# Performance work log

Measured on AMD Instinct MI355X. Metric: run time of the kernel, lower is better.

The kernel has to match this reference:

```python
import jax, jax.numpy as jnp
import numpy as np

E, D, H, TOP_K = 6, 256, 256, 2
ROUTER_H = D // 2  # 128


def setup_inputs() -> dict:
    key = jax.random.key(0)
    ks = jax.random.split(key, 12)
    s = 1.0 / np.sqrt(D)
    sh = 1.0 / np.sqrt(H)
    sr = 1.0 / np.sqrt(ROUTER_H)
    return {
        "features": jax.random.normal(ks[0], (8, 4096, D), dtype=jnp.float32),
        "router_w1": jax.random.uniform(ks[1], (D, ROUTER_H), jnp.float32, -s, s),
        "router_b1": jnp.zeros((ROUTER_H,), jnp.float32),
        "router_w2": jax.random.uniform(ks[2], (ROUTER_H, E), jnp.float32, -sr, sr),
        "router_b2": jnp.zeros((E,), jnp.float32),
        "expert_w1": jax.random.uniform(ks[3], (E, D, H), jnp.float32, -s, s),
        "expert_b1": jnp.zeros((E, H), jnp.float32),
        "expert_w2": jax.random.uniform(ks[4], (E, H, H), jnp.float32, -sh, sh),
        "expert_b2": jnp.zeros((E, H), jnp.float32),
        "expert_w3": jax.random.uniform(ks[5], (E, H, D), jnp.float32, -sh, sh),
        "expert_b3": jnp.zeros((E, D), jnp.float32),
    }


def reference(features, router_w1, router_b1, router_w2, router_b2,
              expert_w1, expert_b1, expert_w2, expert_b2, expert_w3, expert_b3):
    # ---- Router: Linear -> ReLU -> Linear -> Softmax, then top-k + renormalizing softmax
    rh = jax.nn.relu(features @ router_w1 + router_b1)          # [B,S,128]
    expert_logits = jax.nn.softmax(rh @ router_w2 + router_b2, axis=-1)  # [B,S,E]
    top_w, top_i = jax.lax.top_k(expert_logits, TOP_K)          # [B,S,K]
    routing_weights = jax.nn.softmax(top_w, axis=-1)            # [B,S,K]

    # ---- Run ALL experts over all tokens (dense, as in the original)
    h1 = jax.nn.relu(jnp.einsum('bsd,edh->bseh', features, expert_w1) + expert_b1)   # [B,S,E,H]
    h2 = jax.nn.relu(jnp.einsum('bseh,ehf->bsef', h1, expert_w2) + expert_b2)        # [B,S,E,H]
    expert_out = jnp.einsum('bsef,efo->bseo', h2, expert_w3) + expert_b3             # [B,S,E,D]

    # ---- Gather top-k expert outputs and combine with routing weights
    sel = jnp.take_along_axis(expert_out, top_i[:, :, :, None], axis=2)  # [B,S,K,D]
    combined = jnp.sum(sel * routing_weights[..., None], axis=2)         # [B,S,D]
    return combined
```

## Files before the change

### kernel.cpp

```cpp
#include <hip/hip_runtime.h>


#define N_TOK 32768
#define E_EXP 6

typedef _Float16 f16x8 __attribute__((ext_vector_type(8)));
typedef float    f32x4 __attribute__((ext_vector_type(4)));
typedef unsigned int u32x4 __attribute__((ext_vector_type(4)));

#define WS_LIST 256
#define WS_WA   (WS_LIST + 15 * N_TOK * 4)
#define WS_WT   (WS_WA + 15 * N_TOK * 4)
#define WS_R1H  (WS_WT + 2359296)
#define WS_R1L  (WS_R1H + 131072)

__device__ __forceinline__ unsigned pack_f16x2(float x, float y) {
  unsigned short a = __builtin_bit_cast(unsigned short, (_Float16)x);
  unsigned short b = __builtin_bit_cast(unsigned short, (_Float16)y);
  return (unsigned)a | ((unsigned)b << 16);
}

__device__ __forceinline__ void split_pair(float x, float y,
                                           unsigned& hi, unsigned& lo) {
  _Float16 xh = (_Float16)x, yh = (_Float16)y;
  float xl = (x - (float)xh) * 2048.f, yl = (y - (float)yh) * 2048.f;
  hi = (unsigned)__builtin_bit_cast(unsigned short, xh) |
       ((unsigned)__builtin_bit_cast(unsigned short, yh) << 16);
  lo = pack_f16x2(xl, yl);
}

__global__ __launch_bounds__(256) void convert_w_kernel(
    const float* __restrict__ w1, const float* __restrict__ w2,
    const float* __restrict__ w3, const float* __restrict__ rw1,
    _Float16* __restrict__ wt, _Float16* __restrict__ r1h,
    _Float16* __restrict__ r1l, int* __restrict__ counts) {
  __shared__ __align__(16) float xs[32 * 256];
  int blk = blockIdx.x;
  int t = threadIdx.x;
  if (blk == 0 && t < 16) counts[t] = 0;
  float4* xs4 = (float4*)xs;
  if (blk < 144) {
    int kt = blk & 7, el = blk >> 3, l = el % 3, e = el / 3;
    const float* W = (l == 0 ? w1 : (l == 1 ? w2 : w3)) +
                     (size_t)e * 65536 + (size_t)kt * 32 * 256;
    const float4* s4 = (const float4*)W;
    #pragma unroll
    for (int j = 0; j < 8; ++j) xs4[j * 256 + t] = s4[j * 256 + t];
    __syncthreads();
    _Float16* dst = wt + ((size_t)(e * 3 + l) * 8 + kt) * 8192;
    #pragma unroll
    for (int si = 0; si < 4; ++si) {
      int S = si * 256 + t;
      int Ls = S & 63;
      int n = ((S >> 6) << 4) + (Ls & 15);
      int qq = Ls >> 4;
      u32x4 pk;
      #pragma unroll
      for (int i = 0; i < 4; ++i) {
        float x = xs[(qq * 8 + 2 * i) * 256 + n];
        float y = xs[(qq * 8 + 2 * i + 1) * 256 + n];
        pk[i] = pack_f16x2(x, y);
      }
      *(u32x4*)(dst + S * 8) = pk;
    }
  } else {
    int kt = blk - 144;
    const float4* s4 = (const float4*)(rw1 + (size_t)kt * 32 * 128);
    #pragma unroll
    for (int j = 0; j < 4; ++j) xs4[j * 256 + t] = s4[j * 256 + t];
    __syncthreads();
    #pragma unroll
    for (int si = 0; si < 2; ++si) {
      int S = si * 256 + t;
      int Ls = S & 63;
      int n = ((S >> 6) << 4) + (Ls & 15);
      int qq = Ls >> 4;
      u32x4 ph, pl;
      #pragma unroll
      for (int i = 0; i < 4; ++i) {
        float x = xs[(qq * 8 + 2 * i) * 128 + n];
        float y = xs[(qq * 8 + 2 * i + 1) * 128 + n];
        unsigned hi, lo;
        split_pair(x, y, hi, lo);
        ph[i] = hi; pl[i] = lo;
      }
      size_t off = (size_t)kt * 4096 + S * 8;
      *(u32x4*)(r1h + off) = ph;
      *(u32x4*)(r1l + off) = pl;
    }
  }
}

__global__ __launch_bounds__(256) void router_kernel(
    const float* __restrict__ feat, const _Float16* __restrict__ r1h,
    const _Float16* __restrict__ r1l, const float* __restrict__ rb1,
    const float* __restrict__ rw2, const float* __restrict__ rb2,
    int* __restrict__ counts, int* __restrict__ list,
    float* __restrict__ wA) {
  __shared__ __align__(16) char smem[65536];
  __shared__ float plg[64 * 25];
  __shared__ int lcnt[15], gbase[15];
  _Float16* Ahi = (_Float16*)smem;
  _Float16* Alo = (_Float16*)(smem + 32768);
  float* rh = (float*)smem;

  int tid = threadIdx.x;
  int wv = tid >> 6, L = tid & 63, m = L & 15, q = L >> 4;
  int tok0 = blockIdx.x * 64;

  {
    int row = tid >> 2, seg = tid & 3;
    int rt = row >> 4, mm = row & 15;
    const float4* src = (const float4*)(feat + (size_t)(tok0 + row) * 256 + seg * 64);
    #pragma unroll
    for (int i = 0; i < 8; ++i) {
      float4 a = src[2 * i], b = src[2 * i + 1];
      u32x4 ph, pl;
      unsigned h0, l0;
      split_pair(a.x, a.y, h0, l0); ph[0] = h0; pl[0] = l0;
      split_pair(a.z, a.w, h0, l0); ph[1] = h0; pl[1] = l0;
      split_pair(b.x, b.y, h0, l0); ph[2] = h0; pl[2] = l0;
      split_pair(b.z, b.w, h0, l0); ph[3] = h0; pl[3] = l0;
      int k = seg * 64 + i * 8;
      int off = (((k >> 5) * 4 + rt) * 64 + ((k >> 3) & 3) * 16 + mm) * 8;
      *(u32x4*)(Ahi + off) = ph;
      *(u32x4*)(Alo + off) = pl;
    }
  }
  if (tid < 15) lcnt[tid] = 0;

  auto ldH = [&](int kt, int ct) -> f16x8 {
    return *(const f16x8*)(r1h + ((kt * 8 + wv * 2 + ct) * 64 + L) * 8);
  };
  auto ldL = [&](int kt, int ct) -> f16x8 {
    return *(const f16x8*)(r1l + ((kt * 8 + wv * 2 + ct) * 64 + L) * 8);
  };
  f16x8 bch[2], bcl[2];
  #pragma unroll
  for (int ct = 0; ct < 2; ++ct) { bch[ct] = ldH(0, ct); bcl[ct] = ldL(0, ct); }
  __syncthreads();

  f32x4 ach[4][2], acm[4][2];
  #pragma unroll
  for (int ct = 0; ct < 2; ++ct) {
    float bv = rb1[wv * 32 + ct * 16 + m];
    #pragma unroll
    for (int rt = 0; rt < 4; ++rt) {
      ach[rt][ct][0] = bv; ach[rt][ct][1] = bv;
      ach[rt][ct][2] = bv; ach[rt][ct][3] = bv;
      acm[rt][ct][0] = 0.f; acm[rt][ct][1] = 0.f;
      acm[rt][ct][2] = 0.f; acm[rt][ct][3] = 0.f;
    }
  }
  #pragma unroll
  for (int kt = 0; kt < 8; ++kt) {
    f16x8 bnh[2], bnl[2];
    if (kt < 7) {
      #pragma unroll
      for (int ct = 0; ct < 2; ++ct) { bnh[ct] = ldH(kt + 1, ct); bnl[ct] = ldL(kt + 1, ct); }
    }
    f16x8 ah[4], al[4];
    #pragma unroll
    for (int rt = 0; rt < 4; ++rt) {
      ah[rt] = *(const f16x8*)(Ahi + ((kt * 4 + rt) * 64 + L) * 8);
      al[rt] = *(const f16x8*)(Alo + ((kt * 4 + rt) * 64 + L) * 8);
    }
    #pragma unroll
    for (int rt = 0; rt < 4; ++rt)
      #pragma unroll
      for (int ct = 0; ct < 2; ++ct)
        ach[rt][ct] = __builtin_amdgcn_mfma_f32_16x16x32_f16(
            ah[rt], bch[ct], ach[rt][ct], 0, 0, 0);
    #pragma unroll
    for (int rt = 0; rt < 4; ++rt)
      #pragma unroll
      for (int ct = 0; ct < 2; ++ct) {
        acm[rt][ct] = __builtin_amdgcn_mfma_f32_16x16x32_f16(
            ah[rt], bcl[ct], acm[rt][ct], 0, 0, 0);
        acm[rt][ct] = __builtin_amdgcn_mfma_f32_16x16x32_f16(
            al[rt], bch[ct], acm[rt][ct], 0, 0, 0);
      }
    if (kt < 7) {
      #pragma unroll
      for (int ct = 0; ct < 2; ++ct) { bch[ct] = bnh[ct]; bcl[ct] = bnl[ct]; }
    }
  }
  __syncthreads();

  #pragma unroll
  for (int rt = 0; rt < 4; ++rt)
    #pragma unroll
    for (int ct = 0; ct < 2; ++ct)
      #pragma unroll
      for (int r = 0; r < 4; ++r) {
        float v = ach[rt][ct][r] + acm[rt][ct][r] * (1.f / 2048.f);
        int row = rt * 16 + q * 4 + r, h = wv * 32 + ct * 16 + m;
        rh[row * 132 + h] = fmaxf(v, 0.f);
      }
  __syncthreads();

  {
    int t = tid >> 2, sub = tid & 3;
    float lgp[E_EXP] = {0.f, 0.f, 0.f, 0.f, 0.f, 0.f};
    #pragma unroll
    for (int c = 0; c < 8; ++c) {
      int c4 = sub * 8 + c;
      float4 xv = *(const float4*)(rh + t * 132 + c4 * 4);
      #pragma unroll
      for (int j = 0; j < 4; ++j) {
        float xj = (j == 0) ? xv.x : (j == 1) ? xv.y : (j == 2) ? xv.z : xv.w;
        const float* wr = rw2 + (c4 * 4 + j) * E_EXP;
        #pragma unroll
        for (int e2 = 0; e2 < E_EXP; ++e2)
          lgp[e2] = fmaf(xj, wr[e2], lgp[e2]);
      }
    }
    float* pp = plg + t * 25 + sub * 6;
    #pragma unroll
    for (int e2 = 0; e2 < E_EXP; ++e2) pp[e2] = lgp[e2];
  }
  __syncthreads();

  int pid = 0, loc = 0, token = 0;
  float wa = 0.f;
  if (tid < 64) {
    token = tok0 + tid;
    float p[E_EXP];
    float mx = -1e30f;
    #pragma unroll
    for (int i = 0; i < E_EXP; ++i) {
      p[i] = rb2[i] + plg[tid * 25 + i] + plg[tid * 25 + 6 + i] +
             plg[tid * 25 + 12 + i] + plg[tid * 25 + 18 + i];
      mx = fmaxf(mx, p[i]);
    }
    float sum = 0.f;
    #pragma unroll
    for (int i = 0; i < E_EXP; ++i) { p[i] = expf(p[i] - mx); sum += p[i]; }
    float inv = 1.f / sum;
    #pragma unroll
    for (int i = 0; i < E_EXP; ++i) p[i] *= inv;
    float b1v = p[0]; int sel0 = 0;
    #pragma unroll
    for (int i = 1; i < E_EXP; ++i) if (p[i] > b1v) { b1v = p[i]; sel0 = i; }
    float b2v = -1.f; int sel1 = 0;
    #pragma unroll
    for (int i = 0; i < E_EXP; ++i)
      if (i != sel0 && p[i] > b2v) { b2v = p[i]; sel1 = i; }
    float r = expf(b2v - b1v);
    float sw0 = 1.f / (1.f + r);
    float sw1 = r / (1.f + r);
    int a = sel0 < sel1 ? sel0 : sel1;
    int b = sel0 < sel1 ? sel1 : sel0;
    wa = (sel0 < sel1) ? sw0 : sw1;
    pid = b * (b - 1) / 2 + a;
    loc = atomicAdd(&lcnt[pid], 1);
  }
  __syncthreads();
  if (tid < 15) gbase[tid] = atomicAdd(&counts[tid], lcnt[tid]);
  __syncthreads();
  if (tid < 64) {
    int p0 = gbase[pid] + loc;
    list[pid * N_TOK + p0] = token;
    wA[pid * N_TOK + p0] = wa;
  }
}

__global__ __launch_bounds__(256) void expert_kernel(
    const float* __restrict__ feat, const _Float16* __restrict__ wt,
    const float* __restrict__ eb1, const float* __restrict__ eb2,
    const float* __restrict__ eb3, const int* __restrict__ counts,
    const int* __restrict__ list, const float* __restrict__ wA,
    float* __restrict__ out) {
  __shared__ __align__(16) _Float16 Ah[8192];
  __shared__ int   toks[32];
  __shared__ float wgA[32];

  const int loT[15] = {0,0,1,0,1,2,0,1,2,3,0,1,2,3,4};
  const int hiT[15] = {1,2,2,3,3,3,4,4,4,4,5,5,5,5,5};

  int bid = blockIdx.x;
  int pid = 0, tile = 0, cnt = 0, cum = 0;
  #pragma unroll
  for (int i = 0; i < 15; ++i) {
    int ci = counts[i];
    int nt = (ci + 31) >> 5;
    bool hit = (bid >= cum) && (bid < cum + nt);
    if (hit) { pid = i; tile = bid - cum; cnt = ci; }
    cum += nt;
  }
  if (bid >= cum) return;
  int base = tile * 32;
  int eLo = loT[pid], eHi = hiT[pid];

  int tid = threadIdx.x;
  int wv = tid >> 6, L = tid & 63, m = L & 15, q = L >> 4;
  int wcol = wv * 64;

  if (tid < 32) {
    int idx = base + tid;
    int tk = 0; float a = 0.f;
    if (idx < cnt) { tk = list[pid * N_TOK + idx]; a = wA[pid * N_TOK + idx]; }
    toks[tid] = tk; wgA[tid] = a;
  }

  auto ldBs = [&](int s, int ct) -> f16x8 {
    int ee = (s >= 24) ? eHi : eLo;
    int ss = (s >= 24) ? s - 24 : s;
    return *(const f16x8*)(wt + ((size_t)ee * 24 + ss) * 8192 +
                           ((wv * 4 + ct) * 64 + L) * 8);
  };
  f16x8 bc[4], bn[4];
  #pragma unroll
  for (int ct = 0; ct < 4; ++ct) { bc[ct] = ldBs(0, ct); bn[ct] = ldBs(1, ct); }
  __syncthreads();

  f32x4 acc[2][4], accS[2][4];

  #pragma unroll
  for (int pass = 0; pass < 2; ++pass) {
    int e = pass ? eHi : eLo;
    if (pass) __syncthreads();

    {
      int row = tid >> 3, seg = tid & 7;
      int rt = row >> 4, mm = row & 15;
      const float4* src = (const float4*)(feat + (size_t)toks[row] * 256 + seg * 32);
      #pragma unroll
      for (int i = 0; i < 4; ++i) {
        float4 a = src[2 * i], b = src[2 * i + 1];
        u32x4 pk;
        pk[0] = pack_f16x2(a.x, a.y);
        pk[1] = pack_f16x2(a.z, a.w);
        pk[2] = pack_f16x2(b.x, b.y);
        pk[3] = pack_f16x2(b.z, b.w);
        int k = seg * 32 + i * 8;
        int off = (((k >> 5) * 2 + rt) * 64 + ((k >> 3) & 3) * 16 + mm) * 8;
        *(u32x4*)(Ah + off) = pk;
      }
    }
    __syncthreads();

    const float* bias[3] = {eb1 + e * 256, eb2 + e * 256, eb3 + e * 256};

    #pragma unroll
    for (int l = 0; l < 3; ++l) {
      #pragma unroll
      for (int ct = 0; ct < 4; ++ct) {
        float bv = bias[l][wcol + ct * 16 + m];
        #pragma unroll
        for (int rt = 0; rt < 2; ++rt) {
          acc[rt][ct][0] = bv; acc[rt][ct][1] = bv;
          acc[rt][ct][2] = bv; acc[rt][ct][3] = bv;
        }
      }
      #pragma unroll
      for (int kt = 0; kt < 8; ++kt) {
        int s = pass * 24 + l * 8 + kt;
        int sp = (s + 2 <= 47) ? s + 2 : 47;
        f16x8 bn2[4];
        #pragma unroll
        for (int ct = 0; ct < 4; ++ct) bn2[ct] = ldBs(sp, ct);
        f16x8 af[2];
        #pragma unroll
        for (int rt = 0; rt < 2; ++rt)
          af[rt] = *(const f16x8*)(Ah + ((kt * 2 + rt) * 64 + L) * 8);
        #pragma unroll
        for (int rt = 0; rt < 2; ++rt)
          #pragma unroll
          for (int ct = 0; ct < 4; ++ct)
            acc[rt][ct] = __builtin_amdgcn_mfma_f32_16x16x32_f16(
                af[rt], bc[ct], acc[rt][ct], 0, 0, 0);
        #pragma unroll
        for (int ct = 0; ct < 4; ++ct) { bc[ct] = bn[ct]; bn[ct] = bn2[ct]; }
      }
      if (l < 2) {
        __syncthreads();
        int i = m & 3;
        bool s1 = (i & 2) != 0, s2 = (i & 1) != 0;
        #pragma unroll
        for (int rt = 0; rt < 2; ++rt) {
          #pragma unroll
          for (int ct = 0; ct < 4; ++ct) {
            float x0 = acc[rt][ct][0], x1 = acc[rt][ct][1];
            float x2 = acc[rt][ct][2], x3 = acc[rt][ct][3];
            float t0 = __shfl_xor(x2, 2), t1 = __shfl_xor(x3, 2);
            float t2 = __shfl_xor(x0, 2), t3 = __shfl_xor(x1, 2);
            x0 = s1 ? t0 : x0;  x1 = s1 ? t1 : x1;
            x2 = s1 ? x2 : t2;  x3 = s1 ? x3 : t3;
            float u0 = __shfl_xor(x1, 1), u1 = __shfl_xor(x0, 1);
            float u2 = __shfl_xor(x3, 1), u3 = __shfl_xor(x2, 1);
            x0 = s2 ? u0 : x0;  x1 = s2 ? x1 : u1;
            x2 = s2 ? u2 : x2;  x3 = s2 ? x3 : u3;
            uint2 pk;
            pk.x = pack_f16x2(fmaxf(x0, 0.f), fmaxf(x1, 0.f));
            pk.y = pack_f16x2(fmaxf(x2, 0.f), fmaxf(x3, 0.f));
            int n0 = wcol + ct * 16 + (m & ~3);
            int m2 = q * 4 + i;
            int off = (((n0 >> 5) * 2 + rt) * 64 + ((n0 >> 3) & 3) * 16 + m2) * 8 +
                      (n0 & 7);
            *(uint2*)(Ah + off) = pk;
          }
        }
        __syncthreads();
      }
    }

    if (pass == 0) {
      #pragma unroll
      for (int rt = 0; rt < 2; ++rt)
        #pragma unroll
        for (int r = 0; r < 4; ++r) {
          float wa = wgA[rt * 16 + q * 4 + r];
          #pragma unroll
          for (int ct = 0; ct < 4; ++ct)
            accS[rt][ct][r] = acc[rt][ct][r] * wa;
        }
    } else {
      #pragma unroll
      for (int rt = 0; rt < 2; ++rt)
        #pragma unroll
        for (int r = 0; r < 4; ++r) {
          float wb = 1.f - wgA[rt * 16 + q * 4 + r];
          #pragma unroll
          for (int ct = 0; ct < 4; ++ct)
            acc[rt][ct][r] = accS[rt][ct][r] + acc[rt][ct][r] * wb;
        }
    }
  }

  {
    int i = m & 3;
    bool s1 = (i & 2) != 0, s2 = (i & 1) != 0;
    #pragma unroll
    for (int rt = 0; rt < 2; ++rt) {
      int row = rt * 16 + q * 4 + i;
      bool valid = (base + row) < cnt;
      #pragma unroll
      for (int ct = 0; ct < 4; ++ct) {
        float x0 = acc[rt][ct][0], x1 = acc[rt][ct][1];
        float x2 = acc[rt][ct][2], x3 = acc[rt][ct][3];
        float t0 = __shfl_xor(x2, 2), t1 = __shfl_xor(x3, 2);
        float t2 = __shfl_xor(x0, 2), t3 = __shfl_xor(x1, 2);
        x0 = s1 ? t0 : x0;  x1 = s1 ? t1 : x1;
        x2 = s1 ? x2 : t2;  x3 = s1 ? x3 : t3;
        float u0 = __shfl_xor(x1, 1), u1 = __shfl_xor(x0, 1);
        float u2 = __shfl_xor(x3, 1), u3 = __shfl_xor(x2, 1);
        x0 = s2 ? u0 : x0;  x1 = s2 ? x1 : u1;
        x2 = s2 ? u2 : x2;  x3 = s2 ? x3 : u3;
        if (valid) {
          float4 v = make_float4(x0, x1, x2, x3);
          *(float4*)(out + (size_t)toks[row] * 256 + wcol + ct * 16 + (m & ~3)) = v;
        }
      }
    }
  }
}

extern "C" void kernel_launch(void* const* d_in, const int* in_sizes, int n_in,
                              void* d_out, int out_size, void* d_ws, size_t ws_size,
                              hipStream_t stream) {
  const float* feat = (const float*)d_in[0];
  const float* rw1  = (const float*)d_in[1];
  const float* rb1  = (const float*)d_in[2];
  const float* rw2  = (const float*)d_in[3];
  const float* rb2  = (const float*)d_in[4];
  const float* ew1  = (const float*)d_in[5];
  const float* eb1  = (const float*)d_in[6];
  const float* ew2  = (const float*)d_in[7];
  const float* eb2  = (const float*)d_in[8];
  const float* ew3  = (const float*)d_in[9];
  const float* eb3  = (const float*)d_in[10];
  float* out = (float*)d_out;

  char* ws = (char*)d_ws;
  int*      counts = (int*)(ws);
  int*      list   = (int*)(ws + WS_LIST);
  float*    wA     = (float*)(ws + WS_WA);
  _Float16* wt     = (_Float16*)(ws + WS_WT);
  _Float16* r1h    = (_Float16*)(ws + WS_R1H);
  _Float16* r1l    = (_Float16*)(ws + WS_R1L);

  convert_w_kernel<<<152, 256, 0, stream>>>(ew1, ew2, ew3, rw1, wt, r1h, r1l,
                                            counts);
  router_kernel<<<N_TOK / 64, 256, 0, stream>>>(feat, r1h, r1l, rb1, rw2, rb2,
                                                counts, list, wA);
  expert_kernel<<<1039, 256, 0, stream>>>(
      feat, wt, eb1, eb2, eb3, counts, list, wA, out);
}
```

Before: 186.4 us.

## Double expert token tile to 64 and stage weights via async LDS copies

```diff
diff --git a/kernel.cpp b/kernel.cpp
--- a/kernel.cpp
+++ b/kernel.cpp
@@ -27,6 +27,13 @@
   hi = (unsigned)__builtin_bit_cast(unsigned short, xh) |
        ((unsigned)__builtin_bit_cast(unsigned short, yh) << 16);
   lo = pack_f16x2(xl, yl);
+}
+
+__device__ __forceinline__ void async_cp16(const void* g, void* l) {
+  __builtin_amdgcn_global_load_lds(
+      (__attribute__((address_space(1))) void*)(void*)(g),
+      (__attribute__((address_space(3))) void*)(l),
+      16, 0, 0);
 }
 
 __global__ __launch_bounds__(256) void convert_w_kernel(
@@ -265,15 +272,16 @@
   }
 }
 
-__global__ __launch_bounds__(256) void expert_kernel(
+__global__ __launch_bounds__(256, 2) void expert_kernel(
     const float* __restrict__ feat, const _Float16* __restrict__ wt,
     const float* __restrict__ eb1, const float* __restrict__ eb2,
     const float* __restrict__ eb3, const int* __restrict__ counts,
     const int* __restrict__ list, const float* __restrict__ wA,
     float* __restrict__ out) {
-  __shared__ __align__(16) _Float16 Ah[8192];
-  __shared__ int   toks[32];
-  __shared__ float wgA[32];
+  __shared__ __align__(16) _Float16 Ah[16384];
+  __shared__ __align__(16) _Float16 Bh[2][8192];
+  __shared__ int   toks[64];
+  __shared__ float wgA[64];
 
   const int loT[15] = {0,0,1,0,1,2,0,1,2,3,0,1,2,3,4};
   const int hiT[15] = {1,2,2,3,3,3,4,4,4,4,5,5,5,5,5};
@@ -283,63 +291,67 @@
   #pragma unroll
   for (int i = 0; i < 15; ++i) {
     int ci = counts[i];
-    int nt = (ci + 31) >> 5;
+    int nt = (ci + 63) >> 6;
     bool hit = (bid >= cum) && (bid < cum + nt);
     if (hit) { pid = i; tile = bid - cum; cnt = ci; }
     cum += nt;
   }
   if (bid >= cum) return;
-  int base = tile * 32;
+  int base = tile * 64;
   int eLo = loT[pid], eHi = hiT[pid];
 
   int tid = threadIdx.x;
   int wv = tid >> 6, L = tid & 63, m = L & 15, q = L >> 4;
   int wcol = wv * 64;
 
-  if (tid < 32) {
+  if (tid < 64) {
     int idx = base + tid;
     int tk = 0; float a = 0.f;
     if (idx < cnt) { tk = list[pid * N_TOK + idx]; a = wA[pid * N_TOK + idx]; }
     toks[tid] = tk; wgA[tid] = a;
   }
 
-  auto ldBs = [&](int s, int ct) -> f16x8 {
+  auto stageB = [&](int s, int buf) {
     int ee = (s >= 24) ? eHi : eLo;
     int ss = (s >= 24) ? s - 24 : s;
-    return *(const f16x8*)(wt + ((size_t)ee * 24 + ss) * 8192 +
-                           ((wv * 4 + ct) * 64 + L) * 8);
+    const _Float16* src = wt + ((size_t)ee * 24 + ss) * 8192;
+    #pragma unroll
+    for (int j = 0; j < 4; ++j) {
+      int c = j * 256 + tid;
+      async_cp16(src + c * 8, &Bh[buf][c * 8]);
+    }
   };
-  f16x8 bc[4], bn[4];
-  #pragma unroll
-  for (int ct = 0; ct < 4; ++ct) { bc[ct] = ldBs(0, ct); bn[ct] = ldBs(1, ct); }
-  __syncthreads();
-
-  f32x4 acc[2][4], accS[2][4];
+
+  auto stageA = [&]() {
+    int row = tid >> 2, seg = tid & 3;
+    int rt = row >> 4, mm = row & 15;
+    const float* srcr = feat + (size_t)toks[row] * 256 + seg * 64;
+    #pragma unroll
+    for (int i = 0; i < 8; ++i) {
+      int k = seg * 64 + i * 8;
+      float4 a = *(const float4*)(srcr + i * 8);
+      float4 b = *(const float4*)(srcr + i * 8 + 4);
+      u32x4 pk;
+      pk[0] = pack_f16x2(a.x, a.y);
+      pk[1] = pack_f16x2(a.z, a.w);
+      pk[2] = pack_f16x2(b.x, b.y);
+      pk[3] = pack_f16x2(b.z, b.w);
+      int off = (((k >> 5) * 4 + rt) * 64 + ((k >> 3) & 3) * 16 + mm) * 8;
+      *(u32x4*)(Ah + off) = pk;
+    }
+  };
+
+  __syncthreads();
+  stageA();
+  stageB(0, 0);
+  __syncthreads();
+
+  f32x4 acc[4][4], accS[4][4];
+  int s = 0;
 
   #pragma unroll
   for (int pass = 0; pass < 2; ++pass) {
     int e = pass ? eHi : eLo;
-    if (pass) __syncthreads();
-
-    {
-      int row = tid >> 3, seg = tid & 7;
-      int rt = row >> 4, mm = row & 15;
-      const float4* src = (const float4*)(feat + (size_t)toks[row] * 256 + seg * 32);
-      #pragma unroll
-      for (int i = 0; i < 4; ++i) {
-        float4 a = src[2 * i], b = src[2 * i + 1];
-        u32x4 pk;
-        pk[0] = pack_f16x2(a.x, a.y);
-        pk[1] = pack_f16x2(a.z, a.w);
-        pk[2] = pack_f16x2(b.x, b.y);
-        pk[3] = pack_f16x2(b.z, b.w);
-        int k = seg * 32 + i * 8;
-        int off = (((k >> 5) * 2 + rt) * 64 + ((k >> 3) & 3) * 16 + mm) * 8;
-        *(u32x4*)(Ah + off) = pk;
-      }
-    }
-    __syncthreads();
-
     const float* bias[3] = {eb1 + e * 256, eb2 + e * 256, eb3 + e * 256};
 
     #pragma unroll
@@ -348,37 +360,36 @@
       for (int ct = 0; ct < 4; ++ct) {
         float bv = bias[l][wcol + ct * 16 + m];
         #pragma unroll
-        for (int rt = 0; rt < 2; ++rt) {
+        for (int rt = 0; rt < 4; ++rt) {
           acc[rt][ct][0] = bv; acc[rt][ct][1] = bv;
           acc[rt][ct][2] = bv; acc[rt][ct][3] = bv;
         }
       }
       #pragma unroll
-      for (int kt = 0; kt < 8; ++kt) {
-        int s = pass * 24 + l * 8 + kt;
-        int sp = (s + 2 <= 47) ? s + 2 : 47;
-        f16x8 bn2[4];
-        #pragma unroll
-        for (int ct = 0; ct < 4; ++ct) bn2[ct] = ldBs(sp, ct);
-        f16x8 af[2];
-        #pragma unroll
-        for (int rt = 0; rt < 2; ++rt)
-          af[rt] = *(const f16x8*)(Ah + ((kt * 2 + rt) * 64 + L) * 8);
-        #pragma unroll
-        for (int rt = 0; rt < 2; ++rt)
+      for (int kt = 0; kt < 8; ++kt, ++s) {
+        if (s + 1 < 48) stageB(s + 1, (s + 1) & 1);
+        const _Float16* Bb = Bh[s & 1];
+        f16x8 bf[4];
+        #pragma unroll
+        for (int ct = 0; ct < 4; ++ct)
+          bf[ct] = *(const f16x8*)(Bb + ((wv * 4 + ct) * 64 + L) * 8);
+        f16x8 af[4];
+        #pragma unroll
+        for (int rt = 0; rt < 4; ++rt)
+          af[rt] = *(const f16x8*)(Ah + ((kt * 4 + rt) * 64 + L) * 8);
+        #pragma unroll
+        for (int rt = 0; rt < 4; ++rt)
           #pragma unroll
           for (int ct = 0; ct < 4; ++ct)
             acc[rt][ct] = __builtin_amdgcn_mfma_f32_16x16x32_f16(
-                af[rt], bc[ct], acc[rt][ct], 0, 0, 0);
-        #pragma unroll
-        for (int ct = 0; ct < 4; ++ct) { bc[ct] = bn[ct]; bn[ct] = bn2[ct]; }
+                af[rt], bf[ct], acc[rt][ct], 0, 0, 0);
+        __syncthreads();
       }
       if (l < 2) {
-        __syncthreads();
         int i = m & 3;
         bool s1 = (i & 2) != 0, s2 = (i & 1) != 0;
         #pragma unroll
-        for (int rt = 0; rt < 2; ++rt) {
+        for (int rt = 0; rt < 4; ++rt) {
           #pragma unroll
           for (int ct = 0; ct < 4; ++ct) {
             float x0 = acc[rt][ct][0], x1 = acc[rt][ct][1];
@@ -396,7 +407,7 @@
             pk.y = pack_f16x2(fmaxf(x2, 0.f), fmaxf(x3, 0.f));
             int n0 = wcol + ct * 16 + (m & ~3);
             int m2 = q * 4 + i;
-            int off = (((n0 >> 5) * 2 + rt) * 64 + ((n0 >> 3) & 3) * 16 + m2) * 8 +
+            int off = (((n0 >> 5) * 4 + rt) * 64 + ((n0 >> 3) & 3) * 16 + m2) * 8 +
                       (n0 & 7);
             *(uint2*)(Ah + off) = pk;
           }
@@ -407,7 +418,7 @@
 
     if (pass == 0) {
       #pragma unroll
-      for (int rt = 0; rt < 2; ++rt)
+      for (int rt = 0; rt < 4; ++rt)
         #pragma unroll
         for (int r = 0; r < 4; ++r) {
           float wa = wgA[rt * 16 + q * 4 + r];
@@ -415,9 +426,11 @@
           for (int ct = 0; ct < 4; ++ct)
             accS[rt][ct][r] = acc[rt][ct][r] * wa;
         }
+      stageA();
+      __syncthreads();
     } else {
       #pragma unroll
-      for (int rt = 0; rt < 2; ++rt)
+      for (int rt = 0; rt < 4; ++rt)
         #pragma unroll
         for (int r = 0; r < 4; ++r) {
           float wb = 1.f - wgA[rt * 16 + q * 4 + r];
@@ -432,7 +445,7 @@
     int i = m & 3;
     bool s1 = (i & 2) != 0, s2 = (i & 1) != 0;
     #pragma unroll
-    for (int rt = 0; rt < 2; ++rt) {
+    for (int rt = 0; rt < 4; ++rt) {
       int row = rt * 16 + q * 4 + i;
       bool valid = (base + row) < cnt;
       #pragma unroll
@@ -484,6 +497,6 @@
                                             counts);
   router_kernel<<<N_TOK / 64, 256, 0, stream>>>(feat, r1h, r1l, rb1, rw2, rb2,
                                                 counts, list, wA);
-  expert_kernel<<<1039, 256, 0, stream>>>(
+  expert_kernel<<<527, 256, 0, stream>>>(
       feat, wt, eb1, eb2, eb3, counts, list, wA, out);
 }
```

New measurement: 217.4 us. 16.6% more time.

## Shrink router tile, triple-buffer expert weights, load tokens once per pair

Applied to the files above, without the earlier changes.

```diff
diff --git a/kernel.cpp b/kernel.cpp
--- a/kernel.cpp
+++ b/kernel.cpp
@@ -5,6 +5,7 @@
 #define E_EXP 6
 
 typedef _Float16 f16x8 __attribute__((ext_vector_type(8)));
+typedef _Float16 f16x4 __attribute__((ext_vector_type(4)));
 typedef float    f32x4 __attribute__((ext_vector_type(4)));
 typedef unsigned int u32x4 __attribute__((ext_vector_type(4)));
 
@@ -97,23 +98,23 @@
     const float* __restrict__ rw2, const float* __restrict__ rb2,
     int* __restrict__ counts, int* __restrict__ list,
     float* __restrict__ wA) {
-  __shared__ __align__(16) char smem[65536];
-  __shared__ float plg[64 * 25];
+  __shared__ __align__(16) char smem[32768];
+  __shared__ float plg[32 * 49];
   __shared__ int lcnt[15], gbase[15];
   _Float16* Ahi = (_Float16*)smem;
-  _Float16* Alo = (_Float16*)(smem + 32768);
+  _Float16* Alo = (_Float16*)(smem + 16384);
   float* rh = (float*)smem;
 
   int tid = threadIdx.x;
   int wv = tid >> 6, L = tid & 63, m = L & 15, q = L >> 4;
-  int tok0 = blockIdx.x * 64;
+  int tok0 = blockIdx.x * 32;
 
   {
-    int row = tid >> 2, seg = tid & 3;
+    int row = tid >> 3, seg = tid & 7;
     int rt = row >> 4, mm = row & 15;
-    const float4* src = (const float4*)(feat + (size_t)(tok0 + row) * 256 + seg * 64);
-    #pragma unroll
-    for (int i = 0; i < 8; ++i) {
+    const float4* src = (const float4*)(feat + (size_t)(tok0 + row) * 256 + seg * 32);
+    #pragma unroll
+    for (int i = 0; i < 4; ++i) {
       float4 a = src[2 * i], b = src[2 * i + 1];
       u32x4 ph, pl;
       unsigned h0, l0;
@@ -121,8 +122,8 @@
       split_pair(a.z, a.w, h0, l0); ph[1] = h0; pl[1] = l0;
       split_pair(b.x, b.y, h0, l0); ph[2] = h0; pl[2] = l0;
       split_pair(b.z, b.w, h0, l0); ph[3] = h0; pl[3] = l0;
-      int k = seg * 64 + i * 8;
-      int off = (((k >> 5) * 4 + rt) * 64 + ((k >> 3) & 3) * 16 + mm) * 8;
+      int k = seg * 32 + i * 8;
+      int off = (((k >> 5) * 2 + rt) * 64 + ((k >> 3) & 3) * 16 + mm) * 8;
       *(u32x4*)(Ahi + off) = ph;
       *(u32x4*)(Alo + off) = pl;
     }
@@ -140,12 +141,12 @@
   for (int ct = 0; ct < 2; ++ct) { bch[ct] = ldH(0, ct); bcl[ct] = ldL(0, ct); }
   __syncthreads();
 
-  f32x4 ach[4][2], acm[4][2];
+  f32x4 ach[2][2], acm[2][2];
   #pragma unroll
   for (int ct = 0; ct < 2; ++ct) {
     float bv = rb1[wv * 32 + ct * 16 + m];
     #pragma unroll
-    for (int rt = 0; rt < 4; ++rt) {
+    for (int rt = 0; rt < 2; ++rt) {
       ach[rt][ct][0] = bv; ach[rt][ct][1] = bv;
       ach[rt][ct][2] = bv; ach[rt][ct][3] = bv;
       acm[rt][ct][0] = 0.f; acm[rt][ct][1] = 0.f;
@@ -159,22 +160,18 @@
       #pragma unroll
       for (int ct = 0; ct < 2; ++ct) { bnh[ct] = ldH(kt + 1, ct); bnl[ct] = ldL(kt + 1, ct); }
     }
-    f16x8 ah[4], al[4];
-    #pragma unroll
-    for (int rt = 0; rt < 4; ++rt) {
-      ah[rt] = *(const f16x8*)(Ahi + ((kt * 4 + rt) * 64 + L) * 8);
-      al[rt] = *(const f16x8*)(Alo + ((kt * 4 + rt) * 64 + L) * 8);
-    }
-    #pragma unroll
-    for (int rt = 0; rt < 4; ++rt)
-      #pragma unroll
-      for (int ct = 0; ct < 2; ++ct)
+    f16x8 ah[2], al[2];
+    #pragma unroll
+    for (int rt = 0; rt < 2; ++rt) {
+      ah[rt] = *(const f16x8*)(Ahi + ((kt * 2 + rt) * 64 + L) * 8);
+      al[rt] = *(const f16x8*)(Alo + ((kt * 2 + rt) * 64 + L) * 8);
+    }
+    #pragma unroll
+    for (int rt = 0; rt < 2; ++rt)
+      #pragma unroll
+      for (int ct = 0; ct < 2; ++ct) {
         ach[rt][ct] = __builtin_amdgcn_mfma_f32_16x16x32_f16(
             ah[rt], bch[ct], ach[rt][ct], 0, 0, 0);
-    #pragma unroll
-    for (int rt = 0; rt < 4; ++rt)
-      #pragma unroll
-      for (int ct = 0; ct < 2; ++ct) {
         acm[rt][ct] = __builtin_amdgcn_mfma_f32_16x16x32_f16(
             ah[rt], bcl[ct], acm[rt][ct], 0, 0, 0);
         acm[rt][ct] = __builtin_amdgcn_mfma_f32_16x16x32_f16(
@@ -188,7 +185,7 @@
   __syncthreads();
 
   #pragma unroll
-  for (int rt = 0; rt < 4; ++rt)
+  for (int rt = 0; rt < 2; ++rt)
     #pragma unroll
     for (int ct = 0; ct < 2; ++ct)
       #pragma unroll
@@ -200,11 +197,11 @@
   __syncthreads();
 
   {
-    int t = tid >> 2, sub = tid & 3;
+    int t = tid >> 3, sub = tid & 7;
     float lgp[E_EXP] = {0.f, 0.f, 0.f, 0.f, 0.f, 0.f};
     #pragma unroll
-    for (int c = 0; c < 8; ++c) {
-      int c4 = sub * 8 + c;
+    for (int c = 0; c < 4; ++c) {
+      int c4 = sub * 4 + c;
       float4 xv = *(const float4*)(rh + t * 132 + c4 * 4);
       #pragma unroll
       for (int j = 0; j < 4; ++j) {
@@ -215,7 +212,7 @@
           lgp[e2] = fmaf(xj, wr[e2], lgp[e2]);
       }
     }
-    float* pp = plg + t * 25 + sub * 6;
+    float* pp = plg + t * 49 + sub * 6;
     #pragma unroll
     for (int e2 = 0; e2 < E_EXP; ++e2) pp[e2] = lgp[e2];
   }
@@ -223,14 +220,16 @@
 
   int pid = 0, loc = 0, token = 0;
   float wa = 0.f;
-  if (tid < 64) {
+  if (tid < 32) {
     token = tok0 + tid;
     float p[E_EXP];
     float mx = -1e30f;
     #pragma unroll
     for (int i = 0; i < E_EXP; ++i) {
-      p[i] = rb2[i] + plg[tid * 25 + i] + plg[tid * 25 + 6 + i] +
-             plg[tid * 25 + 12 + i] + plg[tid * 25 + 18 + i];
+      float s = rb2[i];
+      #pragma unroll
+      for (int sb = 0; sb < 8; ++sb) s += plg[tid * 49 + sb * 6 + i];
+      p[i] = s;
       mx = fmaxf(mx, p[i]);
     }
     float sum = 0.f;
@@ -258,7 +257,7 @@
   __syncthreads();
   if (tid < 15) gbase[tid] = atomicAdd(&counts[tid], lcnt[tid]);
   __syncthreads();
-  if (tid < 64) {
+  if (tid < 32) {
     int p0 = gbase[pid] + loc;
     list[pid * N_TOK + p0] = token;
     wA[pid * N_TOK + p0] = wa;
@@ -271,7 +270,8 @@
     const float* __restrict__ eb3, const int* __restrict__ counts,
     const int* __restrict__ list, const float* __restrict__ wA,
     float* __restrict__ out) {
-  __shared__ __align__(16) _Float16 Ah[8192];
+  __shared__ __align__(16) _Float16 A0[8192];
+  __shared__ __align__(16) _Float16 Wk[8192];
   __shared__ int   toks[32];
   __shared__ float wgA[32];
 
@@ -296,54 +296,58 @@
   int wv = tid >> 6, L = tid & 63, m = L & 15, q = L >> 4;
   int wcol = wv * 64;
 
-  if (tid < 32) {
-    int idx = base + tid;
-    int tk = 0; float a = 0.f;
-    if (idx < cnt) { tk = list[pid * N_TOK + idx]; a = wA[pid * N_TOK + idx]; }
-    toks[tid] = tk; wgA[tid] = a;
-  }
-
   auto ldBs = [&](int s, int ct) -> f16x8 {
     int ee = (s >= 24) ? eHi : eLo;
     int ss = (s >= 24) ? s - 24 : s;
     return *(const f16x8*)(wt + ((size_t)ee * 24 + ss) * 8192 +
                            ((wv * 4 + ct) * 64 + L) * 8);
   };
-  f16x8 bc[4], bn[4];
-  #pragma unroll
-  for (int ct = 0; ct < 4; ++ct) { bc[ct] = ldBs(0, ct); bn[ct] = ldBs(1, ct); }
-  __syncthreads();
-
-  f32x4 acc[2][4], accS[2][4];
+  f16x8 bq[3][4];
+  #pragma unroll
+  for (int ct = 0; ct < 4; ++ct) {
+    bq[0][ct] = ldBs(0, ct);
+    bq[1][ct] = ldBs(1, ct);
+    bq[2][ct] = ldBs(2, ct);
+  }
+
+  if (tid < 32) {
+    int idx = base + tid;
+    int tk = 0; float a = 0.f;
+    if (idx < cnt) { tk = list[pid * N_TOK + idx]; a = wA[pid * N_TOK + idx]; }
+    toks[tid] = tk; wgA[tid] = a;
+  }
+  __syncthreads();
+
+  {
+    int row = tid >> 3, seg = tid & 7;
+    int rt = row >> 4, mm = row & 15;
+    const float4* src = (const float4*)(feat + (size_t)toks[row] * 256 + seg * 32);
+    #pragma unroll
+    for (int i = 0; i < 4; ++i) {
+      float4 a = src[2 * i], b = src[2 * i + 1];
+      u32x4 pk;
+      pk[0] = pack_f16x2(a.x, a.y);
+      pk[1] = pack_f16x2(a.z, a.w);
+      pk[2] = pack_f16x2(b.x, b.y);
+      pk[3] = pack_f16x2(b.z, b.w);
+      int k = seg * 32 + i * 8;
+      int off = (((k >> 5) * 2 + rt) * 64 + ((k >> 3) & 3) * 16 + mm) * 8;
+      *(u32x4*)(A0 + off) = pk;
+    }
+  }
+  __syncthreads();
+
+  f32x4 acc[2][4];
+  f16x4 accS[2][4];
 
   #pragma unroll
   for (int pass = 0; pass < 2; ++pass) {
     int e = pass ? eHi : eLo;
-    if (pass) __syncthreads();
-
-    {
-      int row = tid >> 3, seg = tid & 7;
-      int rt = row >> 4, mm = row & 15;
-      const float4* src = (const float4*)(feat + (size_t)toks[row] * 256 + seg * 32);
-      #pragma unroll
-      for (int i = 0; i < 4; ++i) {
-        float4 a = src[2 * i], b = src[2 * i + 1];
-        u32x4 pk;
-        pk[0] = pack_f16x2(a.x, a.y);
-        pk[1] = pack_f16x2(a.z, a.w);
-        pk[2] = pack_f16x2(b.x, b.y);
-        pk[3] = pack_f16x2(b.z, b.w);
-        int k = seg * 32 + i * 8;
-        int off = (((k >> 5) * 2 + rt) * 64 + ((k >> 3) & 3) * 16 + mm) * 8;
-        *(u32x4*)(Ah + off) = pk;
-      }
-    }
-    __syncthreads();
-
     const float* bias[3] = {eb1 + e * 256, eb2 + e * 256, eb3 + e * 256};
 
     #pragma unroll
     for (int l = 0; l < 3; ++l) {
+      const _Float16* Asrc = (l == 0) ? A0 : Wk;
       #pragma unroll
       for (int ct = 0; ct < 4; ++ct) {
         float bv = bias[l][wcol + ct * 16 + m];
@@ -356,25 +360,24 @@
       #pragma unroll
       for (int kt = 0; kt < 8; ++kt) {
         int s = pass * 24 + l * 8 + kt;
-        int sp = (s + 2 <= 47) ? s + 2 : 47;
-        f16x8 bn2[4];
-        #pragma unroll
-        for (int ct = 0; ct < 4; ++ct) bn2[ct] = ldBs(sp, ct);
+        int slot = s % 3;
         f16x8 af[2];
         #pragma unroll
         for (int rt = 0; rt < 2; ++rt)
-          af[rt] = *(const f16x8*)(Ah + ((kt * 2 + rt) * 64 + L) * 8);
+          af[rt] = *(const f16x8*)(Asrc + ((kt * 2 + rt) * 64 + L) * 8);
         #pragma unroll
         for (int rt = 0; rt < 2; ++rt)
           #pragma unroll
           for (int ct = 0; ct < 4; ++ct)
             acc[rt][ct] = __builtin_amdgcn_mfma_f32_16x16x32_f16(
-                af[rt], bc[ct], acc[rt][ct], 0, 0, 0);
-        #pragma unroll
-        for (int ct = 0; ct < 4; ++ct) { bc[ct] = bn[ct]; bn[ct] = bn2[ct]; }
+                af[rt], bq[slot][ct], acc[rt][ct], 0, 0, 0);
+        if (s + 3 < 48) {
+          #pragma unroll
+          for (int ct = 0; ct < 4; ++ct) bq[slot][ct] = ldBs(s + 3, ct);
+        }
       }
       if (l < 2) {
-        __syncthreads();
+        if (l == 1) __syncthreads();
         int i = m & 3;
         bool s1 = (i & 2) != 0, s2 = (i & 1) != 0;
         #pragma unroll
@@ -398,7 +401,7 @@
             int m2 = q * 4 + i;
             int off = (((n0 >> 5) * 2 + rt) * 64 + ((n0 >> 3) & 3) * 16 + m2) * 8 +
                       (n0 & 7);
-            *(uint2*)(Ah + off) = pk;
+            *(uint2*)(Wk + off) = pk;
           }
         }
         __syncthreads();
@@ -413,8 +416,9 @@
           float wa = wgA[rt * 16 + q * 4 + r];
           #pragma unroll
           for (int ct = 0; ct < 4; ++ct)
-            accS[rt][ct][r] = acc[rt][ct][r] * wa;
-        }
+            accS[rt][ct][r] = (_Float16)(acc[rt][ct][r] * wa);
+        }
+      __syncthreads();
     } else {
       #pragma unroll
       for (int rt = 0; rt < 2; ++rt)
@@ -423,7 +427,7 @@
           float wb = 1.f - wgA[rt * 16 + q * 4 + r];
           #pragma unroll
           for (int ct = 0; ct < 4; ++ct)
-            acc[rt][ct][r] = accS[rt][ct][r] + acc[rt][ct][r] * wb;
+            acc[rt][ct][r] = (float)accS[rt][ct][r] + acc[rt][ct][r] * wb;
         }
     }
   }
@@ -482,7 +486,7 @@
 
   convert_w_kernel<<<152, 256, 0, stream>>>(ew1, ew2, ew3, rw1, wt, r1h, r1l,
                                             counts);
-  router_kernel<<<N_TOK / 64, 256, 0, stream>>>(feat, r1h, r1l, rb1, rw2, rb2,
+  router_kernel<<<N_TOK / 32, 256, 0, stream>>>(feat, r1h, r1l, rb1, rw2, rb2,
                                                 counts, list, wA);
   expert_kernel<<<1039, 256, 0, stream>>>(
       feat, wt, eb1, eb2, eb3, counts, list, wA, out);
```

Result: faster. 181.7 us (-2.5%).
